# Kernel optimization log

Hardware: AMD Instinct MI355X
Metric: run time of the kernel (lower is better)

Reference implementation:

```python
import jax, jax.numpy as jnp
import numpy as np

N_NODES = 100000
N_EDGES = 3200000
IN_F, HID, OUT = 3, 32, 1
NEG_SLOPE = 0.2


def _glorot(key, shape):
    fan_in, fan_out = shape[0], shape[-1]
    lim = jnp.sqrt(6.0 / (fan_in + fan_out)).astype(jnp.float32)
    return jax.random.uniform(key, shape, jnp.float32, -lim, lim)


def setup_inputs() -> dict:
    key = jax.random.key(0)
    ks = jax.random.split(key, 12)
    x = jax.random.normal(ks[0], (N_NODES, IN_F), jnp.float32)
    edge_index = jax.random.randint(ks[1], (2, N_EDGES), 0, N_NODES, jnp.int32)
    return {
        "x": x,
        "edge_index": edge_index,
        "W1": _glorot(ks[2], (IN_F, HID)),
        "att_src1": _glorot(ks[3], (1, HID))[0],
        "att_dst1": _glorot(ks[4], (1, HID))[0],
        "b1": jnp.zeros((HID,), jnp.float32),
        "W2": _glorot(ks[5], (HID, HID)),
        "att_src2": _glorot(ks[6], (1, HID))[0],
        "att_dst2": _glorot(ks[7], (1, HID))[0],
        "b2": jnp.zeros((HID,), jnp.float32),
        "Wl": _glorot(ks[8], (HID, OUT)),
        "bl": jnp.zeros((OUT,), jnp.float32),
    }


def gat_layer(x, src, dst, W, att_src, att_dst, b):
    # h: [N, HID] dense transform
    h = x @ W
    # per-node attention halves (compute once per node, gather per edge)
    a_s = h @ att_src  # [N]
    a_d = h @ att_dst  # [N]
    logits = jax.nn.leaky_relu(a_s[src] + a_d[dst], NEG_SLOPE)  # [E+N]
    # segment-softmax over incoming edges of each dst node
    m = jax.ops.segment_max(logits, dst, num_segments=N_NODES)
    m = jnp.where(jnp.isfinite(m), m, 0.0)
    ex = jnp.exp(logits - m[dst])
    denom = jax.ops.segment_sum(ex, dst, num_segments=N_NODES)
    coef = ex / (denom[dst] + 1e-16)
    # weighted scatter-aggregate of source messages
    out = jax.ops.segment_sum(coef[:, None] * h[src], dst, num_segments=N_NODES)
    return out + b


def reference(x, edge_index, W1, att_src1, att_dst1, b1, W2, att_src2, att_dst2, b2, Wl, bl):
    # PyG GATConv default: add self-loops
    loops = jnp.arange(N_NODES, dtype=edge_index.dtype)
    src = jnp.concatenate([edge_index[0], loops])
    dst = jnp.concatenate([edge_index[1], loops])
    h = gat_layer(x, src, dst, W1, att_src1, att_dst1, b1)
    h = jax.nn.relu(h)  # dropout is identity in eval
    h = gat_layer(h, src, dst, W2, att_src2, att_dst2, b2)
    h = jax.nn.relu(h)
    return h @ Wl + bl
```

## Files before the change

### kernel.cpp

```cpp
#include <hip/hip_runtime.h>
#include <hip/hip_fp16.h>

#define HID 32
#define BN 132
#define NBPAD 768
#define BSTRIDE 5120
#define CHUNK 4096

__device__ __forceinline__ float lrelu(float x) { return x > 0.0f ? x : 0.2f * x; }

__global__ void k_transform1(const float* __restrict__ x,
                             const float* __restrict__ W1,
                             const float* __restrict__ att_src,
                             const float* __restrict__ att_dst,
                             __half* __restrict__ hh,
                             float* __restrict__ a_s,
                             float* __restrict__ a_d,
                             int* __restrict__ cursor,
                             int N)
{
    int tid = blockIdx.x * blockDim.x + threadIdx.x;
    if (tid < NBPAD) cursor[tid] = 0;
    int n = tid >> 5;
    int f = tid & 31;
    if (n >= N) return;
    float x0 = x[n * 3 + 0], x1 = x[n * 3 + 1], x2 = x[n * 3 + 2];
    float hv = x0 * W1[f] + x1 * W1[HID + f] + x2 * W1[2 * HID + f];
    hh[(size_t)n * HID + f] = __float2half(hv);
    float as = hv * att_src[f];
    float ad = hv * att_dst[f];
    #pragma unroll
    for (int m = 16; m >= 1; m >>= 1) {
        as += __shfl_xor(as, m, 32);
        ad += __shfl_xor(ad, m, 32);
    }
    if (f == 0) { a_s[n] = as; a_d[n] = ad; }
}

__global__ void __launch_bounds__(256) k_binscatter(const int* __restrict__ src,
                                                    const int* __restrict__ dst,
                                                    int* __restrict__ cursor,
                                                    unsigned int* __restrict__ packed,
                                                    int NBr, int E)
{
    __shared__ int stage[CHUNK];
    __shared__ unsigned short sbid[CHUNK];
    __shared__ int lhist[NBPAD], lexcl[NBPAD], lbase[NBPAD], lcur[NBPAD];
    __shared__ int arr[256];
    int t = threadIdx.x;
    for (int i = t; i < NBPAD; i += 256) { lhist[i] = 0; lcur[i] = 0; }
    __syncthreads();
    int base = blockIdx.x * CHUNK;
    int cnt = E - base; if (cnt > CHUNK) cnt = CHUNK;
    for (int i = t; i < cnt; i += 256)
        atomicAdd(&lhist[dst[base + i] / BN], 1);
    __syncthreads();
    int b0 = 3 * t;
    int c0 = lhist[b0], c1 = lhist[b0 + 1], c2 = lhist[b0 + 2];
    int s = c0 + c1 + c2;
    arr[t] = s;
    __syncthreads();
    for (int o = 1; o < 256; o <<= 1) {
        int v = (t >= o) ? arr[t - o] : 0;
        __syncthreads();
        arr[t] += v;
        __syncthreads();
    }
    int ex = arr[t] - s;
    int e0 = ex, e1 = ex + c0, e2 = ex + c0 + c1;
    lexcl[b0] = e0; lexcl[b0 + 1] = e1; lexcl[b0 + 2] = e2;
    for (int i = 0; i < c0; ++i) sbid[e0 + i] = (unsigned short)b0;
    for (int i = 0; i < c1; ++i) sbid[e1 + i] = (unsigned short)(b0 + 1);
    for (int i = 0; i < c2; ++i) sbid[e2 + i] = (unsigned short)(b0 + 2);
    for (int b = t; b < NBr; b += 256)
        if (lhist[b]) lbase[b] = b * BSTRIDE + atomicAdd(&cursor[b], lhist[b]);
    __syncthreads();
    for (int i = t; i < cnt; i += 256) {
        int d = dst[base + i];
        int sv = src[base + i];
        int b = d / BN;
        int dl = d - b * BN;
        int idx = lexcl[b] + atomicAdd(&lcur[b], 1);
        stage[idx] = (int)((unsigned)sv | ((unsigned)dl << 17));
    }
    __syncthreads();
    for (int i = t; i < cnt; i += 256) {
        int b = sbid[i];
        int gpos = lbase[b] + (i - lexcl[b]);
        if (gpos < (b + 1) * BSTRIDE)
            packed[gpos] = (unsigned)stage[i];
    }
}

__device__ __forceinline__ void agg_node(const __half* __restrict__ hh,
                                         const float* __restrict__ a_s,
                                         float a_dn, float a_sn,
                                         const float* __restrict__ b,
                                         int n, int f,
                                         const int* lcsr, int off, int dg,
                                         float& vx, float& vy)
{
    float ex = __expf(lrelu(a_sn + a_dn));
    float den = ex;
    float2 hs = __half22float2(*(const __half2*)(hh + (size_t)n * HID + 2 * f));
    float accx = ex * hs.x;
    float accy = ex * hs.y;
    for (int base = 0; base < dg; base += 16) {
        int m = dg - base; if (m > 16) m = 16;
        int sv = 0;
        float exv = 0.0f;
        if (f < m) {
            sv = lcsr[off + base + f];
            exv = __expf(lrelu(a_s[sv] + a_dn));
        }
        int j = 0;
        for (; j + 8 <= m; j += 8) {
            int s0 = __shfl(sv, j, 16), s1 = __shfl(sv, j + 1, 16);
            int s2 = __shfl(sv, j + 2, 16), s3 = __shfl(sv, j + 3, 16);
            int s4 = __shfl(sv, j + 4, 16), s5 = __shfl(sv, j + 5, 16);
            int s6 = __shfl(sv, j + 6, 16), s7 = __shfl(sv, j + 7, 16);
            float e0 = __shfl(exv, j, 16), e1 = __shfl(exv, j + 1, 16);
            float e2 = __shfl(exv, j + 2, 16), e3 = __shfl(exv, j + 3, 16);
            float e4 = __shfl(exv, j + 4, 16), e5 = __shfl(exv, j + 5, 16);
            float e6 = __shfl(exv, j + 6, 16), e7 = __shfl(exv, j + 7, 16);
            __half2 p0 = *(const __half2*)(hh + (size_t)s0 * HID + 2 * f);
            __half2 p1 = *(const __half2*)(hh + (size_t)s1 * HID + 2 * f);
            __half2 p2 = *(const __half2*)(hh + (size_t)s2 * HID + 2 * f);
            __half2 p3 = *(const __half2*)(hh + (size_t)s3 * HID + 2 * f);
            __half2 p4 = *(const __half2*)(hh + (size_t)s4 * HID + 2 * f);
            __half2 p5 = *(const __half2*)(hh + (size_t)s5 * HID + 2 * f);
            __half2 p6 = *(const __half2*)(hh + (size_t)s6 * HID + 2 * f);
            __half2 p7 = *(const __half2*)(hh + (size_t)s7 * HID + 2 * f);
            float2 q0 = __half22float2(p0), q1 = __half22float2(p1);
            float2 q2 = __half22float2(p2), q3 = __half22float2(p3);
            float2 q4 = __half22float2(p4), q5 = __half22float2(p5);
            float2 q6 = __half22float2(p6), q7 = __half22float2(p7);
            den += ((e0 + e1) + (e2 + e3)) + ((e4 + e5) + (e6 + e7));
            accx = fmaf(e0, q0.x, accx); accy = fmaf(e0, q0.y, accy);
            accx = fmaf(e1, q1.x, accx); accy = fmaf(e1, q1.y, accy);
            accx = fmaf(e2, q2.x, accx); accy = fmaf(e2, q2.y, accy);
            accx = fmaf(e3, q3.x, accx); accy = fmaf(e3, q3.y, accy);
            accx = fmaf(e4, q4.x, accx); accy = fmaf(e4, q4.y, accy);
            accx = fmaf(e5, q5.x, accx); accy = fmaf(e5, q5.y, accy);
            accx = fmaf(e6, q6.x, accx); accy = fmaf(e6, q6.y, accy);
            accx = fmaf(e7, q7.x, accx); accy = fmaf(e7, q7.y, accy);
        }
        for (; j + 4 <= m; j += 4) {
            int s0 = __shfl(sv, j, 16), s1 = __shfl(sv, j + 1, 16);
            int s2 = __shfl(sv, j + 2, 16), s3 = __shfl(sv, j + 3, 16);
            float e0 = __shfl(exv, j, 16), e1 = __shfl(exv, j + 1, 16);
            float e2 = __shfl(exv, j + 2, 16), e3 = __shfl(exv, j + 3, 16);
            __half2 p0 = *(const __half2*)(hh + (size_t)s0 * HID + 2 * f);
            __half2 p1 = *(const __half2*)(hh + (size_t)s1 * HID + 2 * f);
            __half2 p2 = *(const __half2*)(hh + (size_t)s2 * HID + 2 * f);
            __half2 p3 = *(const __half2*)(hh + (size_t)s3 * HID + 2 * f);
            float2 q0 = __half22float2(p0), q1 = __half22float2(p1);
            float2 q2 = __half22float2(p2), q3 = __half22float2(p3);
            den += (e0 + e1) + (e2 + e3);
            accx = fmaf(e0, q0.x, accx); accy = fmaf(e0, q0.y, accy);
            accx = fmaf(e1, q1.x, accx); accy = fmaf(e1, q1.y, accy);
            accx = fmaf(e2, q2.x, accx); accy = fmaf(e2, q2.y, accy);
            accx = fmaf(e3, q3.x, accx); accy = fmaf(e3, q3.y, accy);
        }
        for (; j < m; ++j) {
            int s0 = __shfl(sv, j, 16);
            float e0 = __shfl(exv, j, 16);
            float2 q0 = __half22float2(*(const __half2*)(hh + (size_t)s0 * HID + 2 * f));
            den += e0;
            accx = fmaf(e0, q0.x, accx);
            accy = fmaf(e0, q0.y, accy);
        }
    }
    float inv = 1.0f / (den + 1e-16f);
    vx = fmaxf(accx * inv + b[2 * f], 0.0f);
    vy = fmaxf(accy * inv + b[2 * f + 1], 0.0f);
}

__device__ __forceinline__ void build_lcsr(const unsigned int* pk, int cnt,
                                           int* lcsr, int* lhist, int* lscan, int* lcur)
{
    int t = threadIdx.x;
    if (t < 256) { lhist[t] = 0; lcur[t] = 0; }
    __syncthreads();
    for (int i = t; i < cnt; i += 1024)
        atomicAdd(&lhist[(pk[i] >> 17) & 255], 1);
    __syncthreads();
    if (t < 256) lscan[t] = lhist[t];
    __syncthreads();
    for (int o = 1; o < 256; o <<= 1) {
        int v = (t < 256 && t >= o) ? lscan[t - o] : 0;
        __syncthreads();
        if (t < 256) lscan[t] += v;
        __syncthreads();
    }
    for (int i = t; i < cnt; i += 1024) {
        unsigned int p = pk[i];
        int dl = (p >> 17) & 255;
        int pos = atomicAdd(&lcur[dl], 1);
        lcsr[(lscan[dl] - lhist[dl]) + pos] = (int)(p & 0x1FFFF);
    }
    __syncthreads();
}

__global__ void __launch_bounds__(1024) k_agg_mid_f(const __half* __restrict__ hh,
                          const float* __restrict__ a_s,
                          const float* __restrict__ a_d,
                          const int* __restrict__ cursor,
                          const unsigned int* __restrict__ packed,
                          const float* __restrict__ b1,
                          const float* __restrict__ W2,
                          const float* __restrict__ as2w,
                          const float* __restrict__ ad2w,
                          __half* __restrict__ hh_out,
                          float* __restrict__ as_out,
                          float* __restrict__ ad_out,
                          int N)
{
    __shared__ int lcsr[BSTRIDE];
    __shared__ int lhist[256], lscan[256], lcur[256];
    int bk = blockIdx.x, t = threadIdx.x;
    int cnt = cursor[bk]; if (cnt > BSTRIDE) cnt = BSTRIDE;
    build_lcsr(packed + (size_t)bk * BSTRIDE, cnt, lcsr, lhist, lscan, lcur);
    int g = t >> 4, f = t & 15;
    for (int dl = g; dl < BN; dl += 64) {
        int n = bk * BN + dl;
        if (n >= N) continue;
        int off = lscan[dl] - lhist[dl];
        int dg = lhist[dl];
        float vx, vy;
        agg_node(hh, a_s, a_d[n], a_s[n], b1, n, f, lcsr, off, dg, vx, vy);
        float hx = 0.0f, hy = 0.0f;
        #pragma unroll
        for (int k = 0; k < 16; ++k) {
            float va = __shfl(vx, k, 16);
            float vb = __shfl(vy, k, 16);
            float2 w0 = *(const float2*)(W2 + (2 * k) * HID + 2 * f);
            float2 w1 = *(const float2*)(W2 + (2 * k + 1) * HID + 2 * f);
            hx = fmaf(va, w0.x, hx); hy = fmaf(va, w0.y, hy);
            hx = fmaf(vb, w1.x, hx); hy = fmaf(vb, w1.y, hy);
        }
        *(__half2*)(hh_out + (size_t)n * HID + 2 * f) = __floats2half2_rn(hx, hy);
        float as = hx * as2w[2 * f] + hy * as2w[2 * f + 1];
        float ad = hx * ad2w[2 * f] + hy * ad2w[2 * f + 1];
        #pragma unroll
        for (int m2 = 8; m2 >= 1; m2 >>= 1) {
            as += __shfl_xor(as, m2, 16);
            ad += __shfl_xor(ad, m2, 16);
        }
        if (f == 0) { as_out[n] = as; ad_out[n] = ad; }
    }
}

__global__ void __launch_bounds__(1024) k_agg_out_f(const __half* __restrict__ hh,
                          const float* __restrict__ a_s,
                          const float* __restrict__ a_d,
                          const int* __restrict__ cursor,
                          const unsigned int* __restrict__ packed,
                          const float* __restrict__ b2,
                          const float* __restrict__ Wl,
                          const float* __restrict__ bl,
                          float* __restrict__ out,
                          int N)
{
    __shared__ int lcsr[BSTRIDE];
    __shared__ int lhist[256], lscan[256], lcur[256];
    int bk = blockIdx.x, t = threadIdx.x;
    int cnt = cursor[bk]; if (cnt > BSTRIDE) cnt = BSTRIDE;
    build_lcsr(packed + (size_t)bk * BSTRIDE, cnt, lcsr, lhist, lscan, lcur);
    int g = t >> 4, f = t & 15;
    for (int dl = g; dl < BN; dl += 64) {
        int n = bk * BN + dl;
        if (n >= N) continue;
        int off = lscan[dl] - lhist[dl];
        int dg = lhist[dl];
        float vx, vy;
        agg_node(hh, a_s, a_d[n], a_s[n], b2, n, f, lcsr, off, dg, vx, vy);
        float y = vx * Wl[2 * f] + vy * Wl[2 * f + 1];
        #pragma unroll
        for (int m2 = 8; m2 >= 1; m2 >>= 1)
            y += __shfl_xor(y, m2, 16);
        if (f == 0) out[n] = y + bl[0];
    }
}

extern "C" void kernel_launch(void* const* d_in, const int* in_sizes, int n_in,
                              void* d_out, int out_size, void* d_ws, size_t ws_size,
                              hipStream_t stream)
{
    const float* x        = (const float*)d_in[0];
    const int*   eidx     = (const int*)d_in[1];
    const float* W1       = (const float*)d_in[2];
    const float* att_src1 = (const float*)d_in[3];
    const float* att_dst1 = (const float*)d_in[4];
    const float* b1       = (const float*)d_in[5];
    const float* W2       = (const float*)d_in[6];
    const float* att_src2 = (const float*)d_in[7];
    const float* att_dst2 = (const float*)d_in[8];
    const float* b2       = (const float*)d_in[9];
    const float* Wl       = (const float*)d_in[10];
    const float* bl       = (const float*)d_in[11];
    float* out = (float*)d_out;

    int N = in_sizes[0] / 3;
    int E = in_sizes[1] / 2;
    const int* src = eidx;
    const int* dst = eidx + E;
    int NBr = (N + BN - 1) / BN;

    size_t szNHh = (size_t)N * HID * 2;
    size_t szN4  = (size_t)N * 4;
    size_t szPK  = (size_t)NBr * BSTRIDE * 4;

    char* ws = (char*)d_ws;
    __half* h1h    = (__half*)ws; ws += szNHh;
    __half* h2h    = (__half*)ws; ws += szNHh;
    unsigned int* packed = (unsigned int*)ws; ws += szPK;
    float*  a_s1   = (float*)ws;  ws += szN4;
    float*  a_d1   = (float*)ws;  ws += szN4;
    float*  a_s2   = (float*)ws;  ws += szN4;
    float*  a_d2   = (float*)ws;  ws += szN4;
    int*    cursor = (int*)ws;    ws += NBPAD * 4;

    const int B = 256;
    int gridNode32 = (N * HID + B - 1) / B;
    int gridBin    = (E + CHUNK - 1) / CHUNK;

    k_transform1<<<gridNode32, B, 0, stream>>>(x, W1, att_src1, att_dst1,
                                               h1h, a_s1, a_d1, cursor, N);
    k_binscatter<<<gridBin, B, 0, stream>>>(src, dst, cursor, packed, NBr, E);
    k_agg_mid_f<<<NBr, 1024, 0, stream>>>(h1h, a_s1, a_d1, cursor, packed,
                                          b1, W2, att_src2, att_dst2,
                                          h2h, a_s2, a_d2, N);
    k_agg_out_f<<<NBr, 1024, 0, stream>>>(h2h, a_s2, a_d2, cursor, packed,
                                          b2, Wl, bl, out, N);
}
```

Measured before the change: 275.0 us.

## Split each destination bin across two 256-thread blocks for aggregation

Each aggregation kernel now launches two 256-thread blocks per destination bin instead of one 1024-thread block. Each block handles half of the bin's 132 nodes and builds a local CSR only for its half. This cuts shared memory and block size per block, which should raise occupancy and load balance across CUs. The cost is that every packed edge of a bin is read and filtered twice, and only 16 node groups run per block instead of 64.

```diff
diff --git a/kernel.cpp b/kernel.cpp
--- a/kernel.cpp
+++ b/kernel.cpp
@@ -3,6 +3,8 @@
 
 #define HID 32
 #define BN 132
+#define HBN 66
+#define HCAP 2816
 #define NBPAD 768
 #define BSTRIDE 5120
 #define CHUNK 4096
@@ -176,33 +178,39 @@
     vy = fmaxf(accy * inv + b[2 * f + 1], 0.0f);
 }
 
-__device__ __forceinline__ void build_lcsr(const unsigned int* pk, int cnt,
-                                           int* lcsr, int* lhist, int* lscan, int* lcur)
+__device__ __forceinline__ void build_half_lcsr(const unsigned int* pk, int cnt,
+                                                int halfBase,
+                                                int* lcsr, int* lhist,
+                                                int* lscan, int* lcur)
 {
     int t = threadIdx.x;
-    if (t < 256) { lhist[t] = 0; lcur[t] = 0; }
-    __syncthreads();
-    for (int i = t; i < cnt; i += 1024)
-        atomicAdd(&lhist[(pk[i] >> 17) & 255], 1);
-    __syncthreads();
-    if (t < 256) lscan[t] = lhist[t];
-    __syncthreads();
-    for (int o = 1; o < 256; o <<= 1) {
-        int v = (t < 256 && t >= o) ? lscan[t - o] : 0;
+    if (t < 128) { lhist[t] = 0; lcur[t] = 0; }
+    __syncthreads();
+    for (int i = t; i < cnt; i += 256) {
+        int rel = (int)((pk[i] >> 17) & 255) - halfBase;
+        if ((unsigned)rel < (unsigned)HBN) atomicAdd(&lhist[rel], 1);
+    }
+    __syncthreads();
+    if (t < 128) lscan[t] = lhist[t];
+    __syncthreads();
+    for (int o = 1; o < 128; o <<= 1) {
+        int v = (t < 128 && t >= o) ? lscan[t - o] : 0;
         __syncthreads();
-        if (t < 256) lscan[t] += v;
+        if (t < 128) lscan[t] += v;
         __syncthreads();
     }
-    for (int i = t; i < cnt; i += 1024) {
+    for (int i = t; i < cnt; i += 256) {
         unsigned int p = pk[i];
-        int dl = (p >> 17) & 255;
-        int pos = atomicAdd(&lcur[dl], 1);
-        lcsr[(lscan[dl] - lhist[dl]) + pos] = (int)(p & 0x1FFFF);
-    }
-    __syncthreads();
-}
-
-__global__ void __launch_bounds__(1024) k_agg_mid_f(const __half* __restrict__ hh,
+        int rel = (int)((p >> 17) & 255) - halfBase;
+        if ((unsigned)rel < (unsigned)HBN) {
+            int pos = atomicAdd(&lcur[rel], 1);
+            lcsr[(lscan[rel] - lhist[rel]) + pos] = (int)(p & 0x1FFFF);
+        }
+    }
+    __syncthreads();
+}
+
+__global__ void __launch_bounds__(256) k_agg_mid_f(const __half* __restrict__ hh,
                           const float* __restrict__ a_s,
                           const float* __restrict__ a_d,
                           const int* __restrict__ cursor,
@@ -216,14 +224,17 @@
                           float* __restrict__ ad_out,
                           int N)
 {
-    __shared__ int lcsr[BSTRIDE];
-    __shared__ int lhist[256], lscan[256], lcur[256];
-    int bk = blockIdx.x, t = threadIdx.x;
+    __shared__ int lcsr[HCAP];
+    __shared__ int lhist[128], lscan[128], lcur[128];
+    int bk = blockIdx.x >> 1;
+    int halfBase = (blockIdx.x & 1) * HBN;
+    int t = threadIdx.x;
     int cnt = cursor[bk]; if (cnt > BSTRIDE) cnt = BSTRIDE;
-    build_lcsr(packed + (size_t)bk * BSTRIDE, cnt, lcsr, lhist, lscan, lcur);
+    build_half_lcsr(packed + (size_t)bk * BSTRIDE, cnt, halfBase,
+                    lcsr, lhist, lscan, lcur);
     int g = t >> 4, f = t & 15;
-    for (int dl = g; dl < BN; dl += 64) {
-        int n = bk * BN + dl;
+    for (int dl = g; dl < HBN; dl += 16) {
+        int n = bk * BN + halfBase + dl;
         if (n >= N) continue;
         int off = lscan[dl] - lhist[dl];
         int dg = lhist[dl];
@@ -251,7 +262,7 @@
     }
 }
 
-__global__ void __launch_bounds__(1024) k_agg_out_f(const __half* __restrict__ hh,
+__global__ void __launch_bounds__(256) k_agg_out_f(const __half* __restrict__ hh,
                           const float* __restrict__ a_s,
                           const float* __restrict__ a_d,
                           const int* __restrict__ cursor,
@@ -262,14 +273,17 @@
                           float* __restrict__ out,
                           int N)
 {
-    __shared__ int lcsr[BSTRIDE];
-    __shared__ int lhist[256], lscan[256], lcur[256];
-    int bk = blockIdx.x, t = threadIdx.x;
+    __shared__ int lcsr[HCAP];
+    __shared__ int lhist[128], lscan[128], lcur[128];
+    int bk = blockIdx.x >> 1;
+    int halfBase = (blockIdx.x & 1) * HBN;
+    int t = threadIdx.x;
     int cnt = cursor[bk]; if (cnt > BSTRIDE) cnt = BSTRIDE;
-    build_lcsr(packed + (size_t)bk * BSTRIDE, cnt, lcsr, lhist, lscan, lcur);
+    build_half_lcsr(packed + (size_t)bk * BSTRIDE, cnt, halfBase,
+                    lcsr, lhist, lscan, lcur);
     int g = t >> 4, f = t & 15;
-    for (int dl = g; dl < BN; dl += 64) {
-        int n = bk * BN + dl;
+    for (int dl = g; dl < HBN; dl += 16) {
+        int n = bk * BN + halfBase + dl;
         if (n >= N) continue;
         int off = lscan[dl] - lhist[dl];
         int dg = lhist[dl];
@@ -328,9 +342,9 @@
     k_transform1<<<gridNode32, B, 0, stream>>>(x, W1, att_src1, att_dst1,
                                                h1h, a_s1, a_d1, cursor, N);
     k_binscatter<<<gridBin, B, 0, stream>>>(src, dst, cursor, packed, NBr, E);
-    k_agg_mid_f<<<NBr, 1024, 0, stream>>>(h1h, a_s1, a_d1, cursor, packed,
-                                          b1, W2, att_src2, att_dst2,
-                                          h2h, a_s2, a_d2, N);
-    k_agg_out_f<<<NBr, 1024, 0, stream>>>(h2h, a_s2, a_d2, cursor, packed,
-                                          b2, Wl, bl, out, N);
-}
+    k_agg_mid_f<<<NBr * 2, B, 0, stream>>>(h1h, a_s1, a_d1, cursor, packed,
+                                           b1, W2, att_src2, att_dst2,
+                                           h2h, a_s2, a_d2, N);
+    k_agg_out_f<<<NBr * 2, B, 0, stream>>>(h2h, a_s2, a_d2, cursor, packed,
+                                           b2, Wl, bl, out, N);
+}
```

Result: no change. 272.2 us (-1.0%).
